# Kernel tuning notes

Hardware: AMD Instinct MI355X
Metric: run time of the kernel (lower is better)

## Reference

```python
import jax, jax.numpy as jnp
import numpy as np

C_IN = 12      # total channels (rgb-noised + hidden)
C_NOISE = 3    # noise-prediction channels
HID = 128      # rule-MLP hidden size
PERC = 48      # perception channels (depthwise, 48/12 = 4 filters per channel)
TDIM = 256     # sinusoidal time-embedding dim


def setup_inputs() -> dict:
    key = jax.random.key(0)
    ks = jax.random.split(key, 12)
    B, H, W = 16, 256, 256
    x = jax.random.normal(ks[0], (B, C_NOISE, H, W), jnp.float32)
    hidden_channels = jax.random.normal(ks[1], (B, C_IN - C_NOISE, H, W), jnp.float32)
    t = jax.random.randint(ks[2], (B,), 0, 1000)
    # depthwise 3x3 perceive conv: torch weight shape [out=48, in/groups=1, 3, 3]
    w_perceive = jax.random.normal(ks[3], (PERC, 1, 3, 3), jnp.float32) * 0.1
    b_perceive = jax.random.normal(ks[4], (PERC,), jnp.float32) * 0.01
    # 1x1 convs of the rule network, stored as [out, in]
    w1 = jax.random.normal(ks[5], (HID, PERC), jnp.float32) * 0.1
    b1 = jax.random.normal(ks[6], (HID,), jnp.float32) * 0.01
    w2 = jax.random.normal(ks[7], (HID, HID), jnp.float32) * 0.05
    b2 = jax.random.normal(ks[8], (HID,), jnp.float32) * 0.01
    # conv3 is zero-initialized in the original; random here for test coverage
    w3 = jax.random.normal(ks[9], (C_IN, HID), jnp.float32) * 0.05
    # time embedding Linear(256 -> c_noise)
    w_time = jax.random.normal(ks[10], (C_NOISE, TDIM), jnp.float32) * 0.1
    b_time = jax.random.normal(ks[11], (C_NOISE,), jnp.float32) * 0.01
    return dict(x=x, hidden_channels=hidden_channels, t=t,
                w_perceive=w_perceive, b_perceive=b_perceive,
                w1=w1, b1=b1, w2=w2, b2=b2, w3=w3,
                w_time=w_time, b_time=b_time)


def _pos_encoding(t, channels):
    # t: [B] int -> [B, channels] sinusoidal embedding (torch repeat-then-scale layout)
    inv_freq = 1.0 / (10000.0 ** (jnp.arange(0, channels, 2, dtype=jnp.float32) / channels))
    ang = t.astype(jnp.float32)[:, None] * inv_freq  # [B, channels//2]
    return jnp.concatenate([jnp.sin(ang), jnp.cos(ang)], axis=-1)


def reference(x, hidden_channels, t, w_perceive, b_perceive, w1, b1, w2, b2, w3, w_time, b_time):
    # concat noised channels with hidden state channels -> [B, 12, H, W]
    xf = jnp.concatenate([x, hidden_channels], axis=1)
    # depthwise 3x3 conv, 'same' padding, groups = C_IN
    perc = jax.lax.conv_general_dilated(
        xf, w_perceive, window_strides=(1, 1), padding='SAME',
        feature_group_count=C_IN,
        dimension_numbers=('NCHW', 'OIHW', 'NCHW')) + b_perceive[None, :, None, None]
    # rule network: three 1x1 convs (pointwise MLP) with ReLUs
    h = jax.nn.relu(jnp.einsum('bchw,oc->bohw', perc, w1) + b1[None, :, None, None])
    h = jax.nn.relu(jnp.einsum('bchw,oc->bohw', h, w2) + b2[None, :, None, None])
    out = jnp.einsum('bchw,oc->bohw', h, w3)  # no bias
    # time embedding: sinusoidal -> SiLU -> Linear -> broadcast over H, W
    pe = _pos_encoding(t, TDIM)                       # [B, 256]
    emb = jax.nn.silu(pe) @ w_time.T + b_time         # [B, 3]
    noise_prediction = out[:, :C_NOISE] + emb[:, :, None, None]
    hidden_out = out[:, C_NOISE:]
    return (hidden_out, noise_prediction)
```

## Files before the change

### kernel.cpp

```cpp
#include <hip/hip_runtime.h>


#define ACT_S 136
#define PERC_S 72
#define NOISE_BASE 9437184

#define WSF_OFF 13312
#define WSF_BP 0
#define WSF_B1 48
#define WSF_B2 176
#define WSF_WP 304
#define WSF_EMB 736

typedef short bf16x8 __attribute__((ext_vector_type(8)));
typedef float f32x4 __attribute__((ext_vector_type(4)));

__device__ __forceinline__ short f2bf(float f) {
    union { float f; unsigned u; } cv; cv.f = f;
    unsigned r = cv.u + 0x7FFFu + ((cv.u >> 16) & 1u);
    return (short)(r >> 16);
}
__device__ __forceinline__ unsigned pk2bf(float f0, float f1) {
    union { float f; unsigned u; } a, b; a.f = f0; b.f = f1;
    return __builtin_amdgcn_perm(b.u + 0x8000u, a.u + 0x8000u, 0x07060302u);
}

__global__ void prep_emb_kernel(const float* __restrict__ wpg, const float* __restrict__ bpg,
                                const float* __restrict__ w1g, const float* __restrict__ b1g,
                                const float* __restrict__ w2g, const float* __restrict__ b2g,
                                const float* __restrict__ w3g,
                                const int* __restrict__ t,
                                const float* __restrict__ wt, const float* __restrict__ bt,
                                short* __restrict__ wsb, float* __restrict__ wsf)
{
    if (blockIdx.x < 107) {
        int i = blockIdx.x * 256 + threadIdx.x;
        if (i < 8192) {
            int o = i >> 6, c = i & 63;
            wsb[i] = (c < 48) ? f2bf(w1g[o * 48 + c]) : (short)0;
        } else if (i < 24576) {
            wsb[i] = f2bf(w2g[i - 8192]);
        } else if (i < 26624) {
            int k = i - 24576;
            wsb[i] = (k < 1536) ? f2bf(w3g[k]) : (short)0;
        } else if (i < 26672) {
            wsf[WSF_BP + (i - 26624)] = bpg[i - 26624];
        } else if (i < 26800) {
            wsf[WSF_B1 + (i - 26672)] = b1g[i - 26672];
        } else if (i < 26928) {
            wsf[WSF_B2 + (i - 26800)] = b2g[i - 26800];
        } else if (i < 27360) {
            wsf[WSF_WP + (i - 26928)] = wpg[i - 26928];
        }
        return;
    }
    int b = blockIdx.x - 107;
    int lane = threadIdx.x;
    if (lane >= 64) return;
    float tv = (float)t[b];
    float s0 = 0.f, s1 = 0.f, s2 = 0.f;
    const float LOG1E4 = 9.210340371976184f;
    #pragma unroll
    for (int ii = 0; ii < 2; ++ii) {
        int i = lane + ii * 64;
        float invf = __expf(-LOG1E4 * (float)i * (1.0f / 128.0f));
        float ang = tv * invf;
        float sn = sinf(ang), cs = cosf(ang);
        float ss = sn / (1.0f + __expf(-sn));
        float sc = cs / (1.0f + __expf(-cs));
        s0 += ss * wt[0 * 256 + i] + sc * wt[0 * 256 + i + 128];
        s1 += ss * wt[1 * 256 + i] + sc * wt[1 * 256 + i + 128];
        s2 += ss * wt[2 * 256 + i] + sc * wt[2 * 256 + i + 128];
    }
    #pragma unroll
    for (int off = 32; off; off >>= 1) {
        s0 += __shfl_down(s0, off);
        s1 += __shfl_down(s1, off);
        s2 += __shfl_down(s2, off);
    }
    if (lane == 0) {
        wsf[WSF_EMB + b * 3 + 0] = s0 + bt[0];
        wsf[WSF_EMB + b * 3 + 1] = s1 + bt[1];
        wsf[WSF_EMB + b * 3 + 2] = s2 + bt[2];
    }
}

__global__ __launch_bounds__(256, 3) void canet_main(
    const float* __restrict__ xg,
    const float* __restrict__ hg,
    const short* __restrict__ wsb,
    const float* __restrict__ wsf,
    float* __restrict__ outg)
{
    __shared__ __align__(16) short percS[64 * PERC_S];
    __shared__ __align__(16) short h1S[64 * ACT_S];
    __shared__ __align__(16) short h2S[64 * ACT_S];
    __shared__ __align__(16) float wp_s[48 * 12];
    __shared__ float bp_s[48];

    const int tid = threadIdx.x;
    const int b = blockIdx.x >> 8;
    const int y = blockIdx.x & 255;

    for (int i = tid; i < 576; i += 256) {
        int oc = i / 12, k = i % 12;
        wp_s[i] = (k < 9) ? wsf[WSF_WP + oc * 9 + k] : 0.0f;
    }
    if (tid < 48) bp_s[tid] = wsf[WSF_BP + tid];

    const int wv = tid >> 6;
    const int lane = tid & 63;
    const int m = lane & 15;
    const int q = lane >> 4;

    bf16x8 w1f[2][2], w2f[2][4], w3f[4];
    #pragma unroll
    for (int j = 0; j < 2; ++j) {
        int n = wv * 32 + j * 16 + m;
        #pragma unroll
        for (int ks = 0; ks < 2; ++ks)
            w1f[j][ks] = *(const bf16x8*)(wsb + n * 64 + ks * 32 + q * 8);
        #pragma unroll
        for (int ks = 0; ks < 4; ++ks)
            w2f[j][ks] = *(const bf16x8*)(wsb + 8192 + n * 128 + ks * 32 + q * 8);
    }
    #pragma unroll
    for (int ks = 0; ks < 4; ++ks)
        w3f[ks] = *(const bf16x8*)(wsb + 24576 + m * 128 + ks * 32 + q * 8);

    f32x4 b1v[2], b2v[2];
    #pragma unroll
    for (int j = 0; j < 2; ++j) {
        b1v[j] = *(const f32x4*)(wsf + WSF_B1 + wv * 32 + j * 16 + q * 4);
        b2v[j] = *(const f32x4*)(wsf + WSF_B2 + wv * 32 + j * 16 + q * 4);
    }
    const float embv = (m < 3) ? wsf[WSF_EMB + b * 3 + m] : 0.0f;

    const float* src3[3];
    #pragma unroll
    for (int i3 = 0; i3 < 3; ++i3) {
        int ic = 3 * q + i3;
        src3[i3] = (ic < 3) ? (xg + (((size_t)b * 3 + ic) << 16))
                            : (hg + (((size_t)b * 9 + (ic - 3)) << 16));
    }

    __syncthreads();

    for (int it = 0; it < 4; ++it) {
        const int x0 = it * 64;
        const int px = x0 + wv * 16 + m;

        {
            const int xm1 = px - (px > 0);
            const int xp1 = px + (px < 255);
            const bool okl = (px > 0), okr = (px < 255);
            short* prow = percS + (wv * 16 + m) * PERC_S;
            const bool interior = (y >= 1) && (y <= 254);
            #pragma unroll
            for (int i3 = 0; i3 < 3; ++i3) {
                const float* s = src3[i3];
                float tap[9];
                if (interior) {
                    #pragma unroll
                    for (int ky = 0; ky < 3; ++ky) {
                        const float* rp = s + (y + ky - 1) * 256;
                        float c0 = rp[xm1], c1 = rp[px], c2 = rp[xp1];
                        tap[ky * 3 + 0] = okl ? c0 : 0.0f;
                        tap[ky * 3 + 1] = c1;
                        tap[ky * 3 + 2] = okr ? c2 : 0.0f;
                    }
                } else {
                    #pragma unroll
                    for (int ky = 0; ky < 3; ++ky) {
                        int yy = y + ky - 1;
                        bool yok = (yy >= 0) && (yy < 256);
                        const float* rp = s + (yok ? yy : y) * 256;
                        float c0 = rp[xm1], c1 = rp[px], c2 = rp[xp1];
                        tap[ky * 3 + 0] = (yok && okl) ? c0 : 0.0f;
                        tap[ky * 3 + 1] = yok ? c1 : 0.0f;
                        tap[ky * 3 + 2] = (yok && okr) ? c2 : 0.0f;
                    }
                }
                float v[4];
                #pragma unroll
                for (int r = 0; r < 4; ++r) {
                    int oc = 12 * q + 4 * i3 + r;
                    const float* wrow = &wp_s[oc * 12];
                    f32x4 w0 = *(const f32x4*)wrow;
                    f32x4 w1_ = *(const f32x4*)(wrow + 4);
                    float a = bp_s[oc];
                    a += w0[0] * tap[0] + w0[1] * tap[1] + w0[2] * tap[2] + w0[3] * tap[3];
                    a += w1_[0] * tap[4] + w1_[1] * tap[5] + w1_[2] * tap[6] + w1_[3] * tap[7];
                    a += wrow[8] * tap[8];
                    v[r] = a;
                }
                uint2 pk;
                pk.x = pk2bf(v[0], v[1]);
                pk.y = pk2bf(v[2], v[3]);
                *(uint2*)(prow + 12 * q + 4 * i3) = pk;
            }
            *(uint2*)(prow + 48 + 4 * q) = uint2{0u, 0u};
        }
        __syncthreads();

        #pragma unroll
        for (int nt = 0; nt < 4; ++nt) {
            f32x4 c0 = b1v[0], c1 = b1v[1];
            #pragma unroll
            for (int ks = 0; ks < 2; ++ks) {
                bf16x8 p = *(const bf16x8*)(percS + (nt * 16 + m) * PERC_S + ks * 32 + q * 8);
                c0 = __builtin_amdgcn_mfma_f32_16x16x32_bf16(w1f[0][ks], p, c0, 0, 0, 0);
                c1 = __builtin_amdgcn_mfma_f32_16x16x32_bf16(w1f[1][ks], p, c1, 0, 0, 0);
            }
            short* drow = h1S + (nt * 16 + m) * ACT_S + wv * 32 + q * 4;
            uint2 pk;
            pk.x = pk2bf(fmaxf(c0[0], 0.f), fmaxf(c0[1], 0.f));
            pk.y = pk2bf(fmaxf(c0[2], 0.f), fmaxf(c0[3], 0.f));
            *(uint2*)drow = pk;
            pk.x = pk2bf(fmaxf(c1[0], 0.f), fmaxf(c1[1], 0.f));
            pk.y = pk2bf(fmaxf(c1[2], 0.f), fmaxf(c1[3], 0.f));
            *(uint2*)(drow + 16) = pk;
        }
        __syncthreads();

        #pragma unroll
        for (int nt = 0; nt < 4; ++nt) {
            f32x4 c0 = b2v[0], c1 = b2v[1];
            #pragma unroll
            for (int ks = 0; ks < 4; ++ks) {
                bf16x8 a = *(const bf16x8*)(h1S + (nt * 16 + m) * ACT_S + ks * 32 + q * 8);
                c0 = __builtin_amdgcn_mfma_f32_16x16x32_bf16(w2f[0][ks], a, c0, 0, 0, 0);
                c1 = __builtin_amdgcn_mfma_f32_16x16x32_bf16(w2f[1][ks], a, c1, 0, 0, 0);
            }
            short* drow = h2S + (nt * 16 + m) * ACT_S + wv * 32 + q * 4;
            uint2 pk;
            pk.x = pk2bf(fmaxf(c0[0], 0.f), fmaxf(c0[1], 0.f));
            pk.y = pk2bf(fmaxf(c0[2], 0.f), fmaxf(c0[3], 0.f));
            *(uint2*)drow = pk;
            pk.x = pk2bf(fmaxf(c1[0], 0.f), fmaxf(c1[1], 0.f));
            pk.y = pk2bf(fmaxf(c1[2], 0.f), fmaxf(c1[3], 0.f));
            *(uint2*)(drow + 16) = pk;
        }
        __syncthreads();

        {
            f32x4 acc = {0.f, 0.f, 0.f, 0.f};
            #pragma unroll
            for (int ks = 0; ks < 4; ++ks) {
                bf16x8 a = *(const bf16x8*)(h2S + (wv * 16 + m) * ACT_S + ks * 32 + q * 8);
                acc = __builtin_amdgcn_mfma_f32_16x16x32_bf16(a, w3f[ks], acc, 0, 0, 0);
            }
            if (m < 12) {
                int xx0 = x0 + wv * 16 + q * 4;
                size_t idx;
                if (m < 3) {
                    idx = (size_t)NOISE_BASE + (((size_t)b * 3 + m) << 16) + (size_t)y * 256 + xx0;
                } else {
                    idx = (((size_t)b * 9 + (m - 3)) << 16) + (size_t)y * 256 + xx0;
                }
                f32x4 vst = {acc[0] + embv, acc[1] + embv, acc[2] + embv, acc[3] + embv};
                *(f32x4*)(outg + idx) = vst;
            }
        }
    }
}

extern "C" void kernel_launch(void* const* d_in, const int* in_sizes, int n_in,
                              void* d_out, int out_size, void* d_ws, size_t ws_size,
                              hipStream_t stream) {
    const float* xg  = (const float*)d_in[0];
    const float* hg  = (const float*)d_in[1];
    const int*   tg  = (const int*)  d_in[2];
    const float* wpg = (const float*)d_in[3];
    const float* bpg = (const float*)d_in[4];
    const float* w1g = (const float*)d_in[5];
    const float* b1g = (const float*)d_in[6];
    const float* w2g = (const float*)d_in[7];
    const float* b2g = (const float*)d_in[8];
    const float* w3g = (const float*)d_in[9];
    const float* wtg = (const float*)d_in[10];
    const float* btg = (const float*)d_in[11];
    float* outg = (float*)d_out;
    short* wsb  = (short*)d_ws;
    float* wsf  = (float*)d_ws + WSF_OFF;

    prep_emb_kernel<<<123, 256, 0, stream>>>(wpg, bpg, w1g, b1g, w2g, b2g, w3g,
                                             tg, wtg, btg, wsb, wsf);
    canet_main<<<4096, 256, 0, stream>>>(xg, hg, wsb, wsf, outg);
}
```

Baseline: 224.4 us.

## Fuse weight prep and time embedding into main kernel, drop prep launch

Removes the separate prep kernel. Each block of the main kernel now converts the fp32 weights to bf16 MFMA fragments straight from global memory and computes the sinusoidal time embedding into shared memory. This removes one kernel launch and the serial dependency between the two kernels. In exchange every one of the 4096 blocks repeats the conversion and the embedding math (sin/cos/exp). The change also pads the perceive-weight LDS layout to spread bank accesses, and zeroes the perception padding columns once per block instead of on every iteration.

New measurement: 236.7 us. 5.5% more time.

```diff
diff --git a/kernel.cpp b/kernel.cpp
--- a/kernel.cpp
+++ b/kernel.cpp
@@ -4,13 +4,6 @@
 #define ACT_S 136
 #define PERC_S 72
 #define NOISE_BASE 9437184
-
-#define WSF_OFF 13312
-#define WSF_BP 0
-#define WSF_B1 48
-#define WSF_B2 176
-#define WSF_WP 304
-#define WSF_EMB 736
 
 typedef short bf16x8 __attribute__((ext_vector_type(8)));
 typedef float f32x4 __attribute__((ext_vector_type(4)));
@@ -24,79 +17,38 @@
     union { float f; unsigned u; } a, b; a.f = f0; b.f = f1;
     return __builtin_amdgcn_perm(b.u + 0x8000u, a.u + 0x8000u, 0x07060302u);
 }
-
-__global__ void prep_emb_kernel(const float* __restrict__ wpg, const float* __restrict__ bpg,
-                                const float* __restrict__ w1g, const float* __restrict__ b1g,
-                                const float* __restrict__ w2g, const float* __restrict__ b2g,
-                                const float* __restrict__ w3g,
-                                const int* __restrict__ t,
-                                const float* __restrict__ wt, const float* __restrict__ bt,
-                                short* __restrict__ wsb, float* __restrict__ wsf)
-{
-    if (blockIdx.x < 107) {
-        int i = blockIdx.x * 256 + threadIdx.x;
-        if (i < 8192) {
-            int o = i >> 6, c = i & 63;
-            wsb[i] = (c < 48) ? f2bf(w1g[o * 48 + c]) : (short)0;
-        } else if (i < 24576) {
-            wsb[i] = f2bf(w2g[i - 8192]);
-        } else if (i < 26624) {
-            int k = i - 24576;
-            wsb[i] = (k < 1536) ? f2bf(w3g[k]) : (short)0;
-        } else if (i < 26672) {
-            wsf[WSF_BP + (i - 26624)] = bpg[i - 26624];
-        } else if (i < 26800) {
-            wsf[WSF_B1 + (i - 26672)] = b1g[i - 26672];
-        } else if (i < 26928) {
-            wsf[WSF_B2 + (i - 26800)] = b2g[i - 26800];
-        } else if (i < 27360) {
-            wsf[WSF_WP + (i - 26928)] = wpg[i - 26928];
-        }
-        return;
-    }
-    int b = blockIdx.x - 107;
-    int lane = threadIdx.x;
-    if (lane >= 64) return;
-    float tv = (float)t[b];
-    float s0 = 0.f, s1 = 0.f, s2 = 0.f;
-    const float LOG1E4 = 9.210340371976184f;
-    #pragma unroll
-    for (int ii = 0; ii < 2; ++ii) {
-        int i = lane + ii * 64;
-        float invf = __expf(-LOG1E4 * (float)i * (1.0f / 128.0f));
-        float ang = tv * invf;
-        float sn = sinf(ang), cs = cosf(ang);
-        float ss = sn / (1.0f + __expf(-sn));
-        float sc = cs / (1.0f + __expf(-cs));
-        s0 += ss * wt[0 * 256 + i] + sc * wt[0 * 256 + i + 128];
-        s1 += ss * wt[1 * 256 + i] + sc * wt[1 * 256 + i + 128];
-        s2 += ss * wt[2 * 256 + i] + sc * wt[2 * 256 + i + 128];
-    }
-    #pragma unroll
-    for (int off = 32; off; off >>= 1) {
-        s0 += __shfl_down(s0, off);
-        s1 += __shfl_down(s1, off);
-        s2 += __shfl_down(s2, off);
-    }
-    if (lane == 0) {
-        wsf[WSF_EMB + b * 3 + 0] = s0 + bt[0];
-        wsf[WSF_EMB + b * 3 + 1] = s1 + bt[1];
-        wsf[WSF_EMB + b * 3 + 2] = s2 + bt[2];
-    }
+__device__ __forceinline__ bf16x8 cvt8(const float* __restrict__ p) {
+    f32x4 a = *(const f32x4*)p;
+    f32x4 b = *(const f32x4*)(p + 4);
+    union { unsigned u[4]; bf16x8 v; } r;
+    r.u[0] = pk2bf(a[0], a[1]);
+    r.u[1] = pk2bf(a[2], a[3]);
+    r.u[2] = pk2bf(b[0], b[1]);
+    r.u[3] = pk2bf(b[2], b[3]);
+    return r.v;
 }
 
 __global__ __launch_bounds__(256, 3) void canet_main(
     const float* __restrict__ xg,
     const float* __restrict__ hg,
-    const short* __restrict__ wsb,
-    const float* __restrict__ wsf,
+    const int*   __restrict__ tG,
+    const float* __restrict__ wpg,
+    const float* __restrict__ bpg,
+    const float* __restrict__ w1g,
+    const float* __restrict__ b1g,
+    const float* __restrict__ w2g,
+    const float* __restrict__ b2g,
+    const float* __restrict__ w3g,
+    const float* __restrict__ wtg,
+    const float* __restrict__ btg,
     float* __restrict__ outg)
 {
     __shared__ __align__(16) short percS[64 * PERC_S];
     __shared__ __align__(16) short h1S[64 * ACT_S];
     __shared__ __align__(16) short h2S[64 * ACT_S];
-    __shared__ __align__(16) float wp_s[48 * 12];
+    __shared__ __align__(16) float wp_s[592];
     __shared__ float bp_s[48];
+    __shared__ float embS[4];
 
     const int tid = threadIdx.x;
     const int b = blockIdx.x >> 8;
@@ -104,9 +56,43 @@
 
     for (int i = tid; i < 576; i += 256) {
         int oc = i / 12, k = i % 12;
-        wp_s[i] = (k < 9) ? wsf[WSF_WP + oc * 9 + k] : 0.0f;
-    }
-    if (tid < 48) bp_s[tid] = wsf[WSF_BP + tid];
+        wp_s[i + (oc / 12) * 4] = (k < 9) ? wpg[oc * 9 + k] : 0.0f;
+    }
+    if (tid < 48) bp_s[tid] = bpg[tid];
+
+    {
+        int r = tid >> 2, c = tid & 3;
+        *(uint2*)(percS + r * PERC_S + 48 + c * 4) = uint2{0u, 0u};
+    }
+
+    if (tid < 64) {
+        const float LOG1E4 = 9.210340371976184f;
+        float tv = (float)tG[b];
+        float s0 = 0.f, s1 = 0.f, s2 = 0.f;
+        #pragma unroll
+        for (int ii = 0; ii < 2; ++ii) {
+            int i = tid + ii * 64;
+            float invf = __expf(-LOG1E4 * (float)i * (1.0f / 128.0f));
+            float ang = tv * invf;
+            float sn = sinf(ang), cs = cosf(ang);
+            float ss = sn / (1.0f + __expf(-sn));
+            float sc = cs / (1.0f + __expf(-cs));
+            s0 += ss * wtg[0 * 256 + i] + sc * wtg[0 * 256 + i + 128];
+            s1 += ss * wtg[1 * 256 + i] + sc * wtg[1 * 256 + i + 128];
+            s2 += ss * wtg[2 * 256 + i] + sc * wtg[2 * 256 + i + 128];
+        }
+        #pragma unroll
+        for (int off = 32; off; off >>= 1) {
+            s0 += __shfl_down(s0, off);
+            s1 += __shfl_down(s1, off);
+            s2 += __shfl_down(s2, off);
+        }
+        if (tid == 0) {
+            embS[0] = s0 + btg[0];
+            embS[1] = s1 + btg[1];
+            embS[2] = s2 + btg[2];
+        }
+    }
 
     const int wv = tid >> 6;
     const int lane = tid & 63;
@@ -114,27 +100,26 @@
     const int q = lane >> 4;
 
     bf16x8 w1f[2][2], w2f[2][4], w3f[4];
+    const bf16x8 zfrag = 0;
     #pragma unroll
     for (int j = 0; j < 2; ++j) {
         int n = wv * 32 + j * 16 + m;
-        #pragma unroll
-        for (int ks = 0; ks < 2; ++ks)
-            w1f[j][ks] = *(const bf16x8*)(wsb + n * 64 + ks * 32 + q * 8);
+        w1f[j][0] = cvt8(w1g + n * 48 + q * 8);
+        w1f[j][1] = (q < 2) ? cvt8(w1g + n * 48 + 32 + q * 8) : zfrag;
         #pragma unroll
         for (int ks = 0; ks < 4; ++ks)
-            w2f[j][ks] = *(const bf16x8*)(wsb + 8192 + n * 128 + ks * 32 + q * 8);
+            w2f[j][ks] = cvt8(w2g + n * 128 + ks * 32 + q * 8);
     }
     #pragma unroll
     for (int ks = 0; ks < 4; ++ks)
-        w3f[ks] = *(const bf16x8*)(wsb + 24576 + m * 128 + ks * 32 + q * 8);
+        w3f[ks] = (m < 12) ? cvt8(w3g + m * 128 + ks * 32 + q * 8) : zfrag;
 
     f32x4 b1v[2], b2v[2];
     #pragma unroll
     for (int j = 0; j < 2; ++j) {
-        b1v[j] = *(const f32x4*)(wsf + WSF_B1 + wv * 32 + j * 16 + q * 4);
-        b2v[j] = *(const f32x4*)(wsf + WSF_B2 + wv * 32 + j * 16 + q * 4);
-    }
-    const float embv = (m < 3) ? wsf[WSF_EMB + b * 3 + m] : 0.0f;
+        b1v[j] = *(const f32x4*)(b1g + wv * 32 + j * 16 + q * 4);
+        b2v[j] = *(const f32x4*)(b2g + wv * 32 + j * 16 + q * 4);
+    }
 
     const float* src3[3];
     #pragma unroll
@@ -145,6 +130,8 @@
     }
 
     __syncthreads();
+
+    const float embv = (m < 3) ? embS[m] : 0.0f;
 
     for (int it = 0; it < 4; ++it) {
         const int x0 = it * 64;
@@ -185,7 +172,7 @@
                 #pragma unroll
                 for (int r = 0; r < 4; ++r) {
                     int oc = 12 * q + 4 * i3 + r;
-                    const float* wrow = &wp_s[oc * 12];
+                    const float* wrow = &wp_s[oc * 12 + 4 * q];
                     f32x4 w0 = *(const f32x4*)wrow;
                     f32x4 w1_ = *(const f32x4*)(wrow + 4);
                     float a = bp_s[oc];
@@ -199,7 +186,6 @@
                 pk.y = pk2bf(v[2], v[3]);
                 *(uint2*)(prow + 12 * q + 4 * i3) = pk;
             }
-            *(uint2*)(prow + 48 + 4 * q) = uint2{0u, 0u};
         }
         __syncthreads();
 
@@ -281,10 +267,8 @@
     const float* wtg = (const float*)d_in[10];
     const float* btg = (const float*)d_in[11];
     float* outg = (float*)d_out;
-    short* wsb  = (short*)d_ws;
-    float* wsf  = (float*)d_ws + WSF_OFF;
-
-    prep_emb_kernel<<<123, 256, 0, stream>>>(wpg, bpg, w1g, b1g, w2g, b2g, w3g,
-                                             tg, wtg, btg, wsb, wsf);
-    canet_main<<<4096, 256, 0, stream>>>(xg, hg, wsb, wsf, outg);
-}
+    (void)d_ws; (void)ws_size;
+
+    canet_main<<<4096, 256, 0, stream>>>(xg, hg, tg, wpg, bpg, w1g, b1g, w2g,
+                                         b2g, w3g, wtg, btg, outg);
+}
```
